# Optimization experiments

Measured on AMD Instinct MI355X. Metric: run time of the kernel, lower is better.

The kernel has to match this reference:

```python
import jax, jax.numpy as jnp
import numpy as np

N = 50000
E = 800000
IN_DIM = 256
HID = 64
HEADS = 4
OUT_DIM = 32
NEG_SLOPE = 0.2
EPS = 1e-5


def segment_softmax(logits, seg, num_segments):
    # logits: [E, H]; softmax over edges sharing the same destination node
    m = jax.ops.segment_max(logits, seg, num_segments=num_segments)
    m = jnp.where(jnp.isfinite(m), m, 0.0)
    e = jnp.exp(logits - m[seg])
    s = jax.ops.segment_sum(e, seg, num_segments=num_segments)
    return e / (s[seg] + 1e-16)


def setup_inputs() -> dict:
    key = jax.random.key(0)
    ks = jax.random.split(key, 16)
    d = {}
    d['x'] = jax.random.normal(ks[0], (N, IN_DIM), dtype=jnp.float32)
    d['edge_index'] = jax.random.randint(ks[1], (2, E), 0, N, dtype=jnp.int64)
    sc = lambda fan: 1.0 / np.sqrt(fan)
    # input transform: Linear(256->128), Linear(128->64)
    d['t1_w'] = jax.random.normal(ks[2], (IN_DIM, IN_DIM // 2), dtype=jnp.float32) * sc(IN_DIM)
    d['t1_b'] = jnp.zeros((IN_DIM // 2,), jnp.float32)
    d['t2_w'] = jax.random.normal(ks[3], (IN_DIM // 2, IN_DIM // 4), dtype=jnp.float32) * sc(IN_DIM // 2)
    d['t2_b'] = jnp.zeros((IN_DIM // 4,), jnp.float32)
    d['g1_w'] = jax.random.normal(ks[4], (IN_DIM // 4, HEADS * HID), dtype=jnp.float32) * sc(IN_DIM // 4)
    d['g1_att_src'] = jax.random.normal(ks[5], (HEADS, HID), dtype=jnp.float32) * sc(HID)
    d['g1_att_dst'] = jax.random.normal(ks[6], (HEADS, HID), dtype=jnp.float32) * sc(HID)
    d['g1_b'] = jnp.zeros((HEADS * HID,), jnp.float32)
    # GraphNorm(256)
    d['gn_w'] = jnp.ones((HEADS * HID,), jnp.float32)
    d['gn_b'] = jnp.zeros((HEADS * HID,), jnp.float32)
    d['gn_ms'] = jnp.ones((HEADS * HID,), jnp.float32)
    # GATConv 2: 256 -> 32, 1 head, no concat (mean == identity for 1 head)
    d['g2_w'] = jax.random.normal(ks[7], (HEADS * HID, OUT_DIM), dtype=jnp.float32) * sc(HEADS * HID)
    d['g2_att_src'] = jax.random.normal(ks[8], (1, OUT_DIM), dtype=jnp.float32) * sc(OUT_DIM)
    d['g2_att_dst'] = jax.random.normal(ks[9], (1, OUT_DIM), dtype=jnp.float32) * sc(OUT_DIM)
    d['g2_b'] = jnp.zeros((OUT_DIM,), jnp.float32)
    return d


def gat_conv(x, src, dst, w, att_src, att_dst, bias, n_nodes):
    heads, ch = att_src.shape
    h = (x @ w).reshape(n_nodes, heads, ch)            # [N,H,C]
    a_src = jnp.sum(h * att_src, axis=-1)              # [N,H]
    a_dst = jnp.sum(h * att_dst, axis=-1)              # [N,H]
    logits = jax.nn.leaky_relu(a_src[src] + a_dst[dst], NEG_SLOPE)  # [E,H]
    alpha = segment_softmax(logits, dst, n_nodes)      # [E,H]
    msgs = alpha[:, :, None] * h[src]                  # [E,H,C]
    out = jax.ops.segment_sum(msgs, dst, num_segments=n_nodes)  # [N,H,C]
    return out.reshape(n_nodes, heads * ch) + bias


def reference(x, edge_index, t1_w, t1_b, t2_w, t2_b,
              g1_w, g1_att_src, g1_att_dst, g1_b,
              gn_w, gn_b, gn_ms,
              g2_w, g2_att_src, g2_att_dst, g2_b):
    src, dst = edge_index[0], edge_index[1]
    # input transform (dropout inactive in eval)
    h = jax.nn.relu(x @ t1_w + t1_b)
    h = jax.nn.relu(h @ t2_w + t2_b)
    # GAT layer 1 (concat heads)
    h = gat_conv(h, src, dst, g1_w, g1_att_src, g1_att_dst, g1_b, N)
    # GraphNorm over the whole graph (batch=None -> single graph)
    mean = jnp.mean(h, axis=0)
    o = h - mean * gn_ms
    var = jnp.mean(o * o, axis=0)
    h = o / jnp.sqrt(var + EPS) * gn_w + gn_b
    h = jax.nn.elu(h)
    # GAT layer 2 (1 head, concat=False)
    h = gat_conv(h, src, dst, g2_w, g2_att_src, g2_att_dst, g2_b, N)
    return jax.nn.log_softmax(h, axis=1)
```

## Files before the change

### kernel.cpp

```cpp
#include <hip/hip_runtime.h>

#define NSLOPE 0.2f
#define GEPS 1e-5f

typedef unsigned short ushortT;
typedef __attribute__((ext_vector_type(8))) unsigned short us8;
typedef __attribute__((ext_vector_type(8))) __bf16 bf16x8;
typedef __attribute__((ext_vector_type(4))) float f32x4;

__device__ __forceinline__ float lrelu(float x) { return x >= 0.f ? x : NSLOPE * x; }
__device__ __forceinline__ ushortT f2bf(float f) {
    unsigned int u = __float_as_uint(f);
    return (ushortT)((u + 0x7fffu + ((u >> 16) & 1u)) >> 16);
}
__device__ __forceinline__ float bf2f(ushortT h) {
    return __uint_as_float((unsigned int)h << 16);
}

__global__ __launch_bounds__(256) void k_prep(
    const float* __restrict__ w1, const float* __restrict__ w2,
    const float* __restrict__ g1w, const float* __restrict__ g2w,
    ushortT* __restrict__ w1t, ushortT* __restrict__ w2t,
    ushortT* __restrict__ g1t, ushortT* __restrict__ g2t)
{
    const int i = blockIdx.x * 256 + threadIdx.x;
    if (i < 128 * 256) { const int c = i >> 8, k = i & 255; w1t[i] = f2bf(w1[k * 128 + c]); }
    if (i < 64 * 128)  { const int c = i >> 7, k = i & 127; w2t[i] = f2bf(w2[k * 64 + c]); }
    if (i < 256 * 64)  { const int c = i >> 6, k = i & 63;  g1t[i] = f2bf(g1w[k * 256 + c]); }
    if (i < 32 * 256)  { const int c = i >> 8, k = i & 255; g2t[i] = f2bf(g2w[k * 32 + c]); }
}

__global__ __launch_bounds__(256) void k_lin1(const float* __restrict__ x,
    const ushortT* __restrict__ w1t, const float* __restrict__ b1,
    ushortT* __restrict__ h1, int n)
{
    __shared__ us8 Ab[64 * 128 / 16];
    __shared__ us8 Bb[128 * 128 / 16];
    char* A = (char*)Ab; char* B = (char*)Bb;
    const int t = threadIdx.x;
    const int w = t >> 6, l = t & 63;
    const int lo = l & 15, hi = l >> 4;
    const int n0 = blockIdx.x * 64;
    const int wm = (w >> 1) * 32, wn = (w & 1) * 64;
    f32x4 acc[2][4];
    #pragma unroll
    for (int mf = 0; mf < 2; ++mf)
        #pragma unroll
        for (int nf = 0; nf < 4; ++nf) acc[mf][nf] = (f32x4){0.f, 0.f, 0.f, 0.f};

    const int arow = t >> 2, ak0 = (t & 3) * 16;
    int agn = n0 + arow; if (agn >= n) agn = n - 1;
    const int asw = (arow & 7) << 4;

    for (int kc = 0; kc < 4; ++kc) {
        __syncthreads();
        {
            ushortT tmp[16];
            const float* xp = &x[(size_t)agn * 256 + kc * 64 + ak0];
            #pragma unroll
            for (int j = 0; j < 4; ++j) {
                const float4 v = *(const float4*)(xp + j * 4);
                tmp[j*4+0] = f2bf(v.x); tmp[j*4+1] = f2bf(v.y);
                tmp[j*4+2] = f2bf(v.z); tmp[j*4+3] = f2bf(v.w);
            }
            *(us8*)(A + arow * 128 + ((ak0 * 2) ^ asw)) = *(us8*)tmp;
            *(us8*)(A + arow * 128 + ((ak0 * 2 + 16) ^ asw)) = *(us8*)(tmp + 8);
        }
        #pragma unroll
        for (int i = 0; i < 4; ++i) {
            const int idx = i * 256 + t, br = idx >> 3, bs = idx & 7;
            const us8 v = *(const us8*)&w1t[(size_t)br * 256 + kc * 64 + bs * 8];
            *(us8*)(B + br * 128 + ((bs * 16) ^ ((br & 7) << 4))) = v;
        }
        __syncthreads();
        #pragma unroll
        for (int ks = 0; ks < 2; ++ks) {
            const int koff = ks * 64 + hi * 16;
            bf16x8 af[2], bf[4];
            #pragma unroll
            for (int mf = 0; mf < 2; ++mf) {
                const int r = wm + mf * 16 + lo;
                af[mf] = *(const bf16x8*)(A + r * 128 + (koff ^ ((r & 7) << 4)));
            }
            #pragma unroll
            for (int nf = 0; nf < 4; ++nf) {
                const int r = wn + nf * 16 + lo;
                bf[nf] = *(const bf16x8*)(B + r * 128 + (koff ^ ((r & 7) << 4)));
            }
            #pragma unroll
            for (int mf = 0; mf < 2; ++mf)
                #pragma unroll
                for (int nf = 0; nf < 4; ++nf)
                    acc[mf][nf] = __builtin_amdgcn_mfma_f32_16x16x32_bf16(af[mf], bf[nf], acc[mf][nf], 0, 0, 0);
        }
    }
    #pragma unroll
    for (int nf = 0; nf < 4; ++nf) {
        const int col = wn + nf * 16 + lo;
        const float bb = b1[col];
        #pragma unroll
        for (int mf = 0; mf < 2; ++mf)
            #pragma unroll
            for (int j = 0; j < 4; ++j) {
                const int r = n0 + wm + mf * 16 + hi * 4 + j;
                if (r < n) h1[(size_t)r * 128 + col] = f2bf(fmaxf(acc[mf][nf][j] + bb, 0.f));
            }
    }
}

__global__ __launch_bounds__(256) void k_lin2(const ushortT* __restrict__ h1,
    const ushortT* __restrict__ w2t, const float* __restrict__ b2,
    ushortT* __restrict__ h2, int n)
{
    __shared__ us8 Ab[64 * 128 / 16];
    __shared__ us8 Bb[64 * 128 / 16];
    char* A = (char*)Ab; char* B = (char*)Bb;
    const int t = threadIdx.x;
    const int w = t >> 6, l = t & 63;
    const int lo = l & 15, hi = l >> 4;
    const int n0 = blockIdx.x * 64;
    const int wm = (w >> 1) * 32, wn = (w & 1) * 32;
    f32x4 acc[2][2];
    #pragma unroll
    for (int mf = 0; mf < 2; ++mf)
        #pragma unroll
        for (int nf = 0; nf < 2; ++nf) acc[mf][nf] = (f32x4){0.f, 0.f, 0.f, 0.f};

    const int arow = t >> 2, ak0 = (t & 3) * 16;
    int agn = n0 + arow; if (agn >= n) agn = n - 1;
    const int asw = (arow & 7) << 4;

    for (int kc = 0; kc < 2; ++kc) {
        __syncthreads();
        {
            const us8 v0 = *(const us8*)&h1[(size_t)agn * 128 + kc * 64 + ak0];
            const us8 v1 = *(const us8*)&h1[(size_t)agn * 128 + kc * 64 + ak0 + 8];
            *(us8*)(A + arow * 128 + ((ak0 * 2) ^ asw)) = v0;
            *(us8*)(A + arow * 128 + ((ak0 * 2 + 16) ^ asw)) = v1;
        }
        #pragma unroll
        for (int i = 0; i < 2; ++i) {
            const int idx = i * 256 + t, br = idx >> 3, bs = idx & 7;
            const us8 v = *(const us8*)&w2t[(size_t)br * 128 + kc * 64 + bs * 8];
            *(us8*)(B + br * 128 + ((bs * 16) ^ ((br & 7) << 4))) = v;
        }
        __syncthreads();
        #pragma unroll
        for (int ks = 0; ks < 2; ++ks) {
            const int koff = ks * 64 + hi * 16;
            bf16x8 af[2], bf[2];
            #pragma unroll
            for (int mf = 0; mf < 2; ++mf) {
                const int r = wm + mf * 16 + lo;
                af[mf] = *(const bf16x8*)(A + r * 128 + (koff ^ ((r & 7) << 4)));
            }
            #pragma unroll
            for (int nf = 0; nf < 2; ++nf) {
                const int r = wn + nf * 16 + lo;
                bf[nf] = *(const bf16x8*)(B + r * 128 + (koff ^ ((r & 7) << 4)));
            }
            #pragma unroll
            for (int mf = 0; mf < 2; ++mf)
                #pragma unroll
                for (int nf = 0; nf < 2; ++nf)
                    acc[mf][nf] = __builtin_amdgcn_mfma_f32_16x16x32_bf16(af[mf], bf[nf], acc[mf][nf], 0, 0, 0);
        }
    }
    #pragma unroll
    for (int nf = 0; nf < 2; ++nf) {
        const int col = wn + nf * 16 + lo;
        const float bb = b2[col];
        #pragma unroll
        for (int mf = 0; mf < 2; ++mf)
            #pragma unroll
            for (int j = 0; j < 4; ++j) {
                const int r = n0 + wm + mf * 16 + hi * 4 + j;
                if (r < n) h2[(size_t)r * 64 + col] = f2bf(fmaxf(acc[mf][nf][j] + bb, 0.f));
            }
    }
}

__global__ __launch_bounds__(256) void k_g1feat(const ushortT* __restrict__ h2,
    const ushortT* __restrict__ g1t, const float* __restrict__ attS, const float* __restrict__ attD,
    ushortT* __restrict__ hg1, float* __restrict__ a1s, float* __restrict__ a1d, int n)
{
    __shared__ us8 Ab[64 * 128 / 16];
    __shared__ us8 Bb[256 * 128 / 16];
    char* A = (char*)Ab; char* B = (char*)Bb;
    const int t = threadIdx.x;
    const int w = t >> 6, l = t & 63;
    const int lo = l & 15, hi = l >> 4;
    const int n0 = blockIdx.x * 64;
    const int wm = (w >> 1) * 32, wn = (w & 1) * 128;
    f32x4 acc[2][8];
    #pragma unroll
    for (int mf = 0; mf < 2; ++mf)
        #pragma unroll
        for (int nf = 0; nf < 8; ++nf) acc[mf][nf] = (f32x4){0.f, 0.f, 0.f, 0.f};

    {
        const int arow = t >> 2, ak0 = (t & 3) * 16;
        int agn = n0 + arow; if (agn >= n) agn = n - 1;
        const int asw = (arow & 7) << 4;
        const us8 v0 = *(const us8*)&h2[(size_t)agn * 64 + ak0];
        const us8 v1 = *(const us8*)&h2[(size_t)agn * 64 + ak0 + 8];
        *(us8*)(A + arow * 128 + ((ak0 * 2) ^ asw)) = v0;
        *(us8*)(A + arow * 128 + ((ak0 * 2 + 16) ^ asw)) = v1;
    }
    #pragma unroll
    for (int i = 0; i < 8; ++i) {
        const int idx = i * 256 + t, br = idx >> 3, bs = idx & 7;
        const us8 v = *(const us8*)&g1t[(size_t)br * 64 + bs * 8];
        *(us8*)(B + br * 128 + ((bs * 16) ^ ((br & 7) << 4))) = v;
    }
    __syncthreads();
    #pragma unroll
    for (int ks = 0; ks < 2; ++ks) {
        const int koff = ks * 64 + hi * 16;
        bf16x8 af[2];
        #pragma unroll
        for (int mf = 0; mf < 2; ++mf) {
            const int r = wm + mf * 16 + lo;
            af[mf] = *(const bf16x8*)(A + r * 128 + (koff ^ ((r & 7) << 4)));
        }
        #pragma unroll
        for (int nf = 0; nf < 8; ++nf) {
            const int r = wn + nf * 16 + lo;
            const bf16x8 bf = *(const bf16x8*)(B + r * 128 + (koff ^ ((r & 7) << 4)));
            #pragma unroll
            for (int mf = 0; mf < 2; ++mf)
                acc[mf][nf] = __builtin_amdgcn_mfma_f32_16x16x32_bf16(af[mf], bf, acc[mf][nf], 0, 0, 0);
        }
    }
    float sS[8], sD[8];
    #pragma unroll
    for (int nf = 0; nf < 8; ++nf) {
        sS[nf] = attS[wn + nf * 16 + lo];
        sD[nf] = attD[wn + nf * 16 + lo];
    }
    const int hA = wn >> 6, hB = hA + 1;
    #pragma unroll
    for (int mf = 0; mf < 2; ++mf)
        #pragma unroll
        for (int j = 0; j < 4; ++j) {
            const int r = n0 + wm + mf * 16 + hi * 4 + j;
            float pSA = 0.f, pDA = 0.f, pSB = 0.f, pDB = 0.f;
            #pragma unroll
            for (int nf = 0; nf < 4; ++nf) {
                pSA = fmaf(acc[mf][nf][j], sS[nf], pSA);
                pDA = fmaf(acc[mf][nf][j], sD[nf], pDA);
                pSB = fmaf(acc[mf][nf + 4][j], sS[nf + 4], pSB);
                pDB = fmaf(acc[mf][nf + 4][j], sD[nf + 4], pDB);
            }
            #pragma unroll
            for (int off = 1; off < 16; off <<= 1) {
                pSA += __shfl_xor(pSA, off);
                pDA += __shfl_xor(pDA, off);
                pSB += __shfl_xor(pSB, off);
                pDB += __shfl_xor(pDB, off);
            }
            if (r < n) {
                if (lo == 0) {
                    a1s[r * 4 + hA] = pSA; a1s[r * 4 + hB] = pSB;
                    a1d[r * 4 + hA] = pDA; a1d[r * 4 + hB] = pDB;
                }
                #pragma unroll
                for (int nf = 0; nf < 8; ++nf)
                    hg1[(size_t)r * 256 + wn + nf * 16 + lo] = f2bf(acc[mf][nf][j]);
            }
        }
}

__global__ __launch_bounds__(256) void k_g2feat(const float* __restrict__ out1,
    const float* __restrict__ cscale, const float* __restrict__ cshift,
    const ushortT* __restrict__ g2t, const float* __restrict__ attS, const float* __restrict__ attD,
    ushortT* __restrict__ hg2, float* __restrict__ a2s, float* __restrict__ a2d, int n)
{
    __shared__ us8 Ab[64 * 128 / 16];
    __shared__ us8 Bb[32 * 128 / 16];
    char* A = (char*)Ab; char* B = (char*)Bb;
    const int t = threadIdx.x;
    const int w = t >> 6, l = t & 63;
    const int lo = l & 15, hi = l >> 4;
    const int n0 = blockIdx.x * 64;
    const int wm = w * 16;
    f32x4 acc[2];
    acc[0] = (f32x4){0.f, 0.f, 0.f, 0.f};
    acc[1] = (f32x4){0.f, 0.f, 0.f, 0.f};

    const int arow = t >> 2, ak0 = (t & 3) * 16;
    int agn = n0 + arow; if (agn >= n) agn = n - 1;
    const int asw = (arow & 7) << 4;

    for (int kc = 0; kc < 4; ++kc) {
        __syncthreads();
        {
            ushortT tmp[16];
            const float* xp = &out1[(size_t)agn * 256 + kc * 64 + ak0];
            #pragma unroll
            for (int j = 0; j < 4; ++j) {
                float4 v = *(const float4*)(xp + j * 4);
                const float4 sc = *(const float4*)&cscale[kc * 64 + ak0 + j * 4];
                const float4 sh = *(const float4*)&cshift[kc * 64 + ak0 + j * 4];
                v.x = v.x * sc.x + sh.x; v.y = v.y * sc.y + sh.y;
                v.z = v.z * sc.z + sh.z; v.w = v.w * sc.w + sh.w;
                v.x = v.x > 0.f ? v.x : __expf(v.x) - 1.f;
                v.y = v.y > 0.f ? v.y : __expf(v.y) - 1.f;
                v.z = v.z > 0.f ? v.z : __expf(v.z) - 1.f;
                v.w = v.w > 0.f ? v.w : __expf(v.w) - 1.f;
                tmp[j*4+0] = f2bf(v.x); tmp[j*4+1] = f2bf(v.y);
                tmp[j*4+2] = f2bf(v.z); tmp[j*4+3] = f2bf(v.w);
            }
            *(us8*)(A + arow * 128 + ((ak0 * 2) ^ asw)) = *(us8*)tmp;
            *(us8*)(A + arow * 128 + ((ak0 * 2 + 16) ^ asw)) = *(us8*)(tmp + 8);
        }
        {
            const int br = t >> 3, bs = t & 7;
            const us8 v = *(const us8*)&g2t[(size_t)br * 256 + kc * 64 + bs * 8];
            *(us8*)(B + br * 128 + ((bs * 16) ^ ((br & 7) << 4))) = v;
        }
        __syncthreads();
        #pragma unroll
        for (int ks = 0; ks < 2; ++ks) {
            const int koff = ks * 64 + hi * 16;
            const int ra = wm + lo;
            const bf16x8 af = *(const bf16x8*)(A + ra * 128 + (koff ^ ((ra & 7) << 4)));
            #pragma unroll
            for (int nf = 0; nf < 2; ++nf) {
                const int r = nf * 16 + lo;
                const bf16x8 bf = *(const bf16x8*)(B + r * 128 + (koff ^ ((r & 7) << 4)));
                acc[nf] = __builtin_amdgcn_mfma_f32_16x16x32_bf16(af, bf, acc[nf], 0, 0, 0);
            }
        }
    }
    float sS[2], sD[2];
    sS[0] = attS[lo]; sS[1] = attS[16 + lo];
    sD[0] = attD[lo]; sD[1] = attD[16 + lo];
    #pragma unroll
    for (int j = 0; j < 4; ++j) {
        const int r = n0 + wm + hi * 4 + j;
        float pS = fmaf(acc[0][j], sS[0], acc[1][j] * sS[1]);
        float pD = fmaf(acc[0][j], sD[0], acc[1][j] * sD[1]);
        #pragma unroll
        for (int off = 1; off < 16; off <<= 1) {
            pS += __shfl_xor(pS, off);
            pD += __shfl_xor(pD, off);
        }
        if (r < n) {
            if (lo == 0) { a2s[r] = pS; a2d[r] = pD; }
            hg2[(size_t)r * 32 + lo] = f2bf(acc[0][j]);
            hg2[(size_t)r * 32 + 16 + lo] = f2bf(acc[1][j]);
        }
    }
}

__global__ void k_hist(const int* __restrict__ dst, int* __restrict__ deg, int e) {
    int i = blockIdx.x * 256 + threadIdx.x;
    if (i < e) atomicAdd(&deg[dst[i]], 1);
}

__global__ __launch_bounds__(256) void k_scan1(const int* __restrict__ deg, int* __restrict__ offs,
                                               int* __restrict__ bsum, int n)
{
    __shared__ int sm[256];
    const int t = threadIdx.x;
    const int i = blockIdx.x * 256 + t;
    const int v = (i < n) ? deg[i] : 0;
    sm[t] = v;
    __syncthreads();
    for (int off = 1; off < 256; off <<= 1) {
        int add = (t >= off) ? sm[t - off] : 0;
        __syncthreads();
        sm[t] += add;
        __syncthreads();
    }
    if (i < n) offs[i] = sm[t] - v;
    if (t == 255) bsum[blockIdx.x] = sm[255];
}

__global__ __launch_bounds__(256) void k_scan2(int* __restrict__ bsum, int nb) {
    __shared__ int sm[256];
    const int t = threadIdx.x;
    const int v = (t < nb) ? bsum[t] : 0;
    sm[t] = v;
    __syncthreads();
    for (int off = 1; off < 256; off <<= 1) {
        int add = (t >= off) ? sm[t - off] : 0;
        __syncthreads();
        sm[t] += add;
        __syncthreads();
    }
    if (t < nb) bsum[t] = sm[t] - v;
}

__global__ void k_scan3(int* __restrict__ offs, int* __restrict__ cursor,
                        const int* __restrict__ bsum, int n, int e) {
    int i = blockIdx.x * 256 + threadIdx.x;
    if (i < n) {
        int o = offs[i] + bsum[i >> 8];
        offs[i] = o;
        cursor[i] = o;
    }
    if (i == 0) offs[n] = e;
}

__global__ void k_scatter(const int* __restrict__ src, const int* __restrict__ dst,
                          int* __restrict__ cursor, int* __restrict__ csr, int e) {
    int i = blockIdx.x * 256 + threadIdx.x;
    if (i < e) {
        int p = atomicAdd(&cursor[dst[i]], 1);
        csr[p] = src[i];
    }
}

__global__ __launch_bounds__(256) void k_alpha1(
    const float* __restrict__ a1s, const float* __restrict__ a1d,
    const int* __restrict__ offs, const int* __restrict__ csr,
    float* __restrict__ alphaE, int n)
{
    const int l = threadIdx.x & 15;
    const int d = blockIdx.x * 16 + (threadIdx.x >> 4);
    if (d >= n) return;
    const int start = offs[d], end = offs[d + 1];
    const float4* __restrict__ a1s4 = (const float4*)a1s;
    const float4 adv = ((const float4*)a1d)[d];
    const float ad0 = adv.x, ad1 = adv.y, ad2 = adv.z, ad3 = adv.w;

    float m0 = -1e30f, m1 = -1e30f, m2 = -1e30f, m3 = -1e30f;
    float s0 = 0.f, s1 = 0.f, s2 = 0.f, s3 = 0.f;
    for (int e = start + l; e < end; e += 16) {
        const float4 av = a1s4[csr[e]];
        const float l0 = lrelu(av.x + ad0), l1 = lrelu(av.y + ad1);
        const float l2 = lrelu(av.z + ad2), l3 = lrelu(av.w + ad3);
        float nm;
        nm = fmaxf(m0, l0); s0 = s0 * __expf(m0 - nm) + __expf(l0 - nm); m0 = nm;
        nm = fmaxf(m1, l1); s1 = s1 * __expf(m1 - nm) + __expf(l1 - nm); m1 = nm;
        nm = fmaxf(m2, l2); s2 = s2 * __expf(m2 - nm) + __expf(l2 - nm); m2 = nm;
        nm = fmaxf(m3, l3); s3 = s3 * __expf(m3 - nm) + __expf(l3 - nm); m3 = nm;
    }
    for (int off = 1; off < 16; off <<= 1) {
        float om, os, nm;
        om = __shfl_xor(m0, off, 16); os = __shfl_xor(s0, off, 16);
        nm = fmaxf(m0, om); s0 = s0 * __expf(m0 - nm) + os * __expf(om - nm); m0 = nm;
        om = __shfl_xor(m1, off, 16); os = __shfl_xor(s1, off, 16);
        nm = fmaxf(m1, om); s1 = s1 * __expf(m1 - nm) + os * __expf(om - nm); m1 = nm;
        om = __shfl_xor(m2, off, 16); os = __shfl_xor(s2, off, 16);
        nm = fmaxf(m2, om); s2 = s2 * __expf(m2 - nm) + os * __expf(om - nm); m2 = nm;
        om = __shfl_xor(m3, off, 16); os = __shfl_xor(s3, off, 16);
        nm = fmaxf(m3, om); s3 = s3 * __expf(m3 - nm) + os * __expf(om - nm); m3 = nm;
    }
    const float i0 = 1.f / (s0 + 1e-16f), i1 = 1.f / (s1 + 1e-16f);
    const float i2 = 1.f / (s2 + 1e-16f), i3 = 1.f / (s3 + 1e-16f);
    for (int e = start + l; e < end; e += 16) {
        const float4 av = a1s4[csr[e]];
        float4 o;
        o.x = __expf(lrelu(av.x + ad0) - m0) * i0;
        o.y = __expf(lrelu(av.y + ad1) - m1) * i1;
        o.z = __expf(lrelu(av.z + ad2) - m2) * i2;
        o.w = __expf(lrelu(av.w + ad3) - m3) * i3;
        *(float4*)&alphaE[(size_t)e * 4] = o;
    }
}

__global__ __launch_bounds__(256) void k_pv1(
    const ushortT* __restrict__ hg1, const float* __restrict__ alphaE,
    const int* __restrict__ offs, const int* __restrict__ csr,
    const float* __restrict__ bias, float* __restrict__ out1, int n)
{
    const int lane = threadIdx.x & 63;
    const int d = blockIdx.x * 4 + (threadIdx.x >> 6);
    if (d >= n) return;
    const int start = offs[d], end = offs[d + 1];
    const int c = lane * 4;
    const int head = lane >> 4;
    float acc0 = 0.f, acc1 = 0.f, acc2 = 0.f, acc3 = 0.f;
    #pragma unroll 4
    for (int e = start; e < end; ++e) {
        const int si = csr[e];
        const float al = alphaE[(size_t)e * 4 + head];
        const ushort4 hv = *(const ushort4*)&hg1[(size_t)si * 256 + c];
        acc0 = fmaf(al, bf2f(hv.x), acc0);
        acc1 = fmaf(al, bf2f(hv.y), acc1);
        acc2 = fmaf(al, bf2f(hv.z), acc2);
        acc3 = fmaf(al, bf2f(hv.w), acc3);
    }
    const float4 bv = *(const float4*)&bias[c];
    float4 o = {acc0 + bv.x, acc1 + bv.y, acc2 + bv.z, acc3 + bv.w};
    *(float4*)&out1[(size_t)d * 256 + c] = o;
}

__global__ __launch_bounds__(256) void k_colstat(const float* __restrict__ out1,
    float* __restrict__ colsum, float* __restrict__ colsq, int n)
{
    const int t = threadIdx.x;
    float s = 0.f, q = 0.f;
    for (int r = blockIdx.x; r < n; r += gridDim.x) {
        float v = out1[(size_t)r * 256 + t];
        s += v;
        q += v * v;
    }
    atomicAdd(&colsum[t], s);
    atomicAdd(&colsq[t], q);
}

__global__ void k_norm_params(const float* __restrict__ colsum, const float* __restrict__ colsq,
    const float* __restrict__ gw, const float* __restrict__ gb, const float* __restrict__ gms,
    float* __restrict__ scale, float* __restrict__ shift, int n)
{
    const int t = threadIdx.x;
    const float invn = 1.f / (float)n;
    const float mean = colsum[t] * invn;
    const float msq = colsq[t] * invn;
    const float ms = gms[t];
    const float var = msq - 2.f * ms * mean * mean + ms * ms * mean * mean;
    const float sc = gw[t] * rsqrtf(var + GEPS);
    scale[t] = sc;
    shift[t] = gb[t] - mean * ms * sc;
}

__global__ __launch_bounds__(256) void k_alpha2(
    const float* __restrict__ a2s, const float* __restrict__ a2d,
    const int* __restrict__ offs, const int* __restrict__ csr,
    float* __restrict__ alphaE2, int n)
{
    const int l = threadIdx.x & 15;
    const int d = blockIdx.x * 16 + (threadIdx.x >> 4);
    if (d >= n) return;
    const int start = offs[d], end = offs[d + 1];
    const float adv = a2d[d];
    float m = -1e30f, s = 0.f;
    for (int e = start + l; e < end; e += 16) {
        const float lv = lrelu(a2s[csr[e]] + adv);
        const float nm = fmaxf(m, lv);
        s = s * __expf(m - nm) + __expf(lv - nm);
        m = nm;
    }
    for (int off = 1; off < 16; off <<= 1) {
        const float om = __shfl_xor(m, off, 16), os = __shfl_xor(s, off, 16);
        const float nm = fmaxf(m, om);
        s = s * __expf(m - nm) + os * __expf(om - nm);
        m = nm;
    }
    const float inv = 1.f / (s + 1e-16f);
    for (int e = start + l; e < end; e += 16)
        alphaE2[e] = __expf(lrelu(a2s[csr[e]] + adv) - m) * inv;
}

__global__ __launch_bounds__(256) void k_pv2(
    const ushortT* __restrict__ hg2, const float* __restrict__ alphaE2,
    const int* __restrict__ offs, const int* __restrict__ csr,
    const float* __restrict__ bias, float* __restrict__ out, int n)
{
    const int l = threadIdx.x & 31;
    const int d = blockIdx.x * 8 + (threadIdx.x >> 5);
    if (d >= n) return;
    const int start = offs[d], end = offs[d + 1];
    float acc = 0.f;
    #pragma unroll 4
    for (int e = start; e < end; ++e) {
        const int si = csr[e];
        const float al = alphaE2[e];
        acc = fmaf(al, bf2f(hg2[(size_t)si * 32 + l]), acc);
    }
    const float v = acc + bias[l];
    float mx = v;
    for (int off = 16; off; off >>= 1) mx = fmaxf(mx, __shfl_xor(mx, off, 32));
    float se = __expf(v - mx);
    for (int off = 16; off; off >>= 1) se += __shfl_xor(se, off, 32);
    out[(size_t)d * 32 + l] = v - mx - __logf(se);
}

extern "C" void kernel_launch(void* const* d_in, const int* in_sizes, int n_in,
                              void* d_out, int out_size, void* d_ws, size_t ws_size,
                              hipStream_t stream)
{
    const float* x    = (const float*)d_in[0];
    const int*   ei   = (const int*)d_in[1];
    const float* t1w  = (const float*)d_in[2];
    const float* t1b  = (const float*)d_in[3];
    const float* t2w  = (const float*)d_in[4];
    const float* t2b  = (const float*)d_in[5];
    const float* g1w  = (const float*)d_in[6];
    const float* g1as = (const float*)d_in[7];
    const float* g1ad = (const float*)d_in[8];
    const float* g1b  = (const float*)d_in[9];
    const float* gnw  = (const float*)d_in[10];
    const float* gnb  = (const float*)d_in[11];
    const float* gnms = (const float*)d_in[12];
    const float* g2w  = (const float*)d_in[13];
    const float* g2as = (const float*)d_in[14];
    const float* g2ad = (const float*)d_in[15];
    const float* g2b  = (const float*)d_in[16];

    const int N = in_sizes[0] / 256;
    const int E = in_sizes[1] / 2;
    const int* srcA = ei;
    const int* dstA = ei + E;

    char* ws = (char*)d_ws;
    size_t cur = 0;
    auto alloc = [&](size_t bytes) -> char* {
        char* p = ws + cur;
        cur += (bytes + 255) & ~(size_t)255;
        return p;
    };
    ushortT* h1      = (ushortT*)alloc((size_t)N * 128 * 2);
    ushortT* h2      = (ushortT*)alloc((size_t)N * 64 * 2);
    ushortT* hg1     = (ushortT*)alloc((size_t)N * 256 * 2);
    float*   a1s     = (float*)alloc((size_t)N * 4 * 4);
    float*   a1d     = (float*)alloc((size_t)N * 4 * 4);
    float*   out1    = (float*)alloc((size_t)N * 256 * 4);
    ushortT* hg2     = (ushortT*)alloc((size_t)N * 32 * 2);
    float*   a2s     = (float*)alloc((size_t)N * 4);
    float*   a2d     = (float*)alloc((size_t)N * 4);
    int*     deg     = (int*)alloc((size_t)(N + 1) * 4);
    int*     offs    = (int*)alloc((size_t)(N + 1) * 4);
    int*     cursor  = (int*)alloc((size_t)N * 4);
    int*     bsum    = (int*)alloc(1024);
    int*     csr     = (int*)alloc((size_t)E * 4);
    float*   alphaE  = (float*)alloc((size_t)E * 4 * 4);
    float*   alphaE2 = (float*)alloc((size_t)E * 4);
    float*   colsum  = (float*)alloc(1024);
    float*   colsq   = (float*)alloc(1024);
    float*   cscale  = (float*)alloc(1024);
    float*   cshift  = (float*)alloc(1024);
    ushortT* w1t     = (ushortT*)alloc(128 * 256 * 2);
    ushortT* w2t     = (ushortT*)alloc(64 * 128 * 2);
    ushortT* g1t     = (ushortT*)alloc(256 * 64 * 2);
    ushortT* g2t     = (ushortT*)alloc(32 * 256 * 2);

    hipMemsetAsync(deg, 0, (size_t)(N + 1) * 4, stream);
    hipMemsetAsync(colsum, 0, 2048, stream);

    const int EB  = (E + 255) / 256;
    const int NB  = (N + 255) / 256;
    const int B64 = (N + 63) / 64;
    const int B16 = (N + 15) / 16;
    const int B8  = (N + 7) / 8;
    const int B4  = (N + 3) / 4;

    k_prep<<<128, 256, 0, stream>>>(t1w, t2w, g1w, g2w, w1t, w2t, g1t, g2t);
    k_lin1<<<B64, 256, 0, stream>>>(x, w1t, t1b, h1, N);
    k_lin2<<<B64, 256, 0, stream>>>(h1, w2t, t2b, h2, N);
    k_g1feat<<<B64, 256, 0, stream>>>(h2, g1t, g1as, g1ad, hg1, a1s, a1d, N);
    k_hist<<<EB, 256, 0, stream>>>(dstA, deg, E);
    k_scan1<<<NB, 256, 0, stream>>>(deg, offs, bsum, N);
    k_scan2<<<1, 256, 0, stream>>>(bsum, NB);
    k_scan3<<<NB, 256, 0, stream>>>(offs, cursor, bsum, N, E);
    k_scatter<<<EB, 256, 0, stream>>>(srcA, dstA, cursor, csr, E);
    k_alpha1<<<B16, 256, 0, stream>>>(a1s, a1d, offs, csr, alphaE, N);
    k_pv1<<<B4, 256, 0, stream>>>(hg1, alphaE, offs, csr, g1b, out1, N);
    k_colstat<<<256, 256, 0, stream>>>(out1, colsum, colsq, N);
    k_norm_params<<<1, 256, 0, stream>>>(colsum, colsq, gnw, gnb, gnms, cscale, cshift, N);
    k_g2feat<<<B64, 256, 0, stream>>>(out1, cscale, cshift, g2t, g2as, g2ad, hg2, a2s, a2d, N);
    k_alpha2<<<B16, 256, 0, stream>>>(a2s, a2d, offs, csr, alphaE2, N);
    k_pv2<<<B8, 256, 0, stream>>>(hg2, alphaE2, offs, csr, g2b, (float*)d_out, N);
}
```

Baseline: 324.7 us.

## Store layer-1 GAT output in bf16 and stage edge lists in LDS

The intermediate out1 tensor (N x 256) is now written as bf16 instead of fp32. That halves the bytes written by k_pv1 and read by k_colstat and k_g2feat, and those kernels now convert on load. Separately, k_pv1 and k_pv2 stage chunks of source indices and attention weights into shared memory with one coalesced load per wavefront. This replaces the per-edge scalar broadcast loads from global memory. Rounding out1 to bf16 before GraphNorm statistics adds some precision loss.

```diff
diff --git a/kernel.cpp b/kernel.cpp
--- a/kernel.cpp
+++ b/kernel.cpp
@@ -271,7 +271,7 @@
         }
 }
 
-__global__ __launch_bounds__(256) void k_g2feat(const float* __restrict__ out1,
+__global__ __launch_bounds__(256) void k_g2feat(const ushortT* __restrict__ out1,
     const float* __restrict__ cscale, const float* __restrict__ cshift,
     const ushortT* __restrict__ g2t, const float* __restrict__ attS, const float* __restrict__ attD,
     ushortT* __restrict__ hg2, float* __restrict__ a2s, float* __restrict__ a2d, int n)
@@ -296,20 +296,15 @@
         __syncthreads();
         {
             ushortT tmp[16];
-            const float* xp = &out1[(size_t)agn * 256 + kc * 64 + ak0];
-            #pragma unroll
-            for (int j = 0; j < 4; ++j) {
-                float4 v = *(const float4*)(xp + j * 4);
-                const float4 sc = *(const float4*)&cscale[kc * 64 + ak0 + j * 4];
-                const float4 sh = *(const float4*)&cshift[kc * 64 + ak0 + j * 4];
-                v.x = v.x * sc.x + sh.x; v.y = v.y * sc.y + sh.y;
-                v.z = v.z * sc.z + sh.z; v.w = v.w * sc.w + sh.w;
-                v.x = v.x > 0.f ? v.x : __expf(v.x) - 1.f;
-                v.y = v.y > 0.f ? v.y : __expf(v.y) - 1.f;
-                v.z = v.z > 0.f ? v.z : __expf(v.z) - 1.f;
-                v.w = v.w > 0.f ? v.w : __expf(v.w) - 1.f;
-                tmp[j*4+0] = f2bf(v.x); tmp[j*4+1] = f2bf(v.y);
-                tmp[j*4+2] = f2bf(v.z); tmp[j*4+3] = f2bf(v.w);
+            const us8 v0 = *(const us8*)&out1[(size_t)agn * 256 + kc * 64 + ak0];
+            const us8 v1 = *(const us8*)&out1[(size_t)agn * 256 + kc * 64 + ak0 + 8];
+            #pragma unroll
+            for (int j = 0; j < 8; ++j) {
+                float a = bf2f(v0[j]) * cscale[kc * 64 + ak0 + j] + cshift[kc * 64 + ak0 + j];
+                float b = bf2f(v1[j]) * cscale[kc * 64 + ak0 + 8 + j] + cshift[kc * 64 + ak0 + 8 + j];
+                a = a > 0.f ? a : __expf(a) - 1.f;
+                b = b > 0.f ? b : __expf(b) - 1.f;
+                tmp[j] = f2bf(a); tmp[8 + j] = f2bf(b);
             }
             *(us8*)(A + arow * 128 + ((ak0 * 2) ^ asw)) = *(us8*)tmp;
             *(us8*)(A + arow * 128 + ((ak0 * 2 + 16) ^ asw)) = *(us8*)(tmp + 8);
@@ -465,37 +460,48 @@
 __global__ __launch_bounds__(256) void k_pv1(
     const ushortT* __restrict__ hg1, const float* __restrict__ alphaE,
     const int* __restrict__ offs, const int* __restrict__ csr,
-    const float* __restrict__ bias, float* __restrict__ out1, int n)
-{
-    const int lane = threadIdx.x & 63;
-    const int d = blockIdx.x * 4 + (threadIdx.x >> 6);
+    const float* __restrict__ bias, ushortT* __restrict__ out1, int n)
+{
+    __shared__ int sSid[4][64];
+    __shared__ float sAl[4][256];
+    const int lane = threadIdx.x & 63, w = threadIdx.x >> 6;
+    const int d = blockIdx.x * 4 + w;
     if (d >= n) return;
     const int start = offs[d], end = offs[d + 1];
     const int c = lane * 4;
     const int head = lane >> 4;
     float acc0 = 0.f, acc1 = 0.f, acc2 = 0.f, acc3 = 0.f;
-    #pragma unroll 4
-    for (int e = start; e < end; ++e) {
-        const int si = csr[e];
-        const float al = alphaE[(size_t)e * 4 + head];
-        const ushort4 hv = *(const ushort4*)&hg1[(size_t)si * 256 + c];
-        acc0 = fmaf(al, bf2f(hv.x), acc0);
-        acc1 = fmaf(al, bf2f(hv.y), acc1);
-        acc2 = fmaf(al, bf2f(hv.z), acc2);
-        acc3 = fmaf(al, bf2f(hv.w), acc3);
+    for (int base = start; base < end; base += 64) {
+        const int cnt = min(64, end - base);
+        if (lane < cnt) {
+            sSid[w][lane] = csr[base + lane];
+            *(float4*)&sAl[w][lane * 4] = *(const float4*)&alphaE[(size_t)(base + lane) * 4];
+        }
+        #pragma unroll 8
+        for (int i = 0; i < cnt; ++i) {
+            const int si = sSid[w][i];
+            const float al = sAl[w][i * 4 + head];
+            const ushort4 hv = *(const ushort4*)&hg1[(size_t)si * 256 + c];
+            acc0 = fmaf(al, bf2f(hv.x), acc0);
+            acc1 = fmaf(al, bf2f(hv.y), acc1);
+            acc2 = fmaf(al, bf2f(hv.z), acc2);
+            acc3 = fmaf(al, bf2f(hv.w), acc3);
+        }
     }
     const float4 bv = *(const float4*)&bias[c];
-    float4 o = {acc0 + bv.x, acc1 + bv.y, acc2 + bv.z, acc3 + bv.w};
-    *(float4*)&out1[(size_t)d * 256 + c] = o;
-}
-
-__global__ __launch_bounds__(256) void k_colstat(const float* __restrict__ out1,
+    ushort4 o;
+    o.x = f2bf(acc0 + bv.x); o.y = f2bf(acc1 + bv.y);
+    o.z = f2bf(acc2 + bv.z); o.w = f2bf(acc3 + bv.w);
+    *(ushort4*)&out1[(size_t)d * 256 + c] = o;
+}
+
+__global__ __launch_bounds__(256) void k_colstat(const ushortT* __restrict__ out1,
     float* __restrict__ colsum, float* __restrict__ colsq, int n)
 {
     const int t = threadIdx.x;
     float s = 0.f, q = 0.f;
     for (int r = blockIdx.x; r < n; r += gridDim.x) {
-        float v = out1[(size_t)r * 256 + t];
+        const float v = bf2f(out1[(size_t)r * 256 + t]);
         s += v;
         q += v * v;
     }
@@ -551,16 +557,25 @@
     const int* __restrict__ offs, const int* __restrict__ csr,
     const float* __restrict__ bias, float* __restrict__ out, int n)
 {
-    const int l = threadIdx.x & 31;
-    const int d = blockIdx.x * 8 + (threadIdx.x >> 5);
+    __shared__ int sSid[8][32];
+    __shared__ float sAl[8][32];
+    const int l = threadIdx.x & 31, w = threadIdx.x >> 5;
+    const int d = blockIdx.x * 8 + w;
     if (d >= n) return;
     const int start = offs[d], end = offs[d + 1];
     float acc = 0.f;
-    #pragma unroll 4
-    for (int e = start; e < end; ++e) {
-        const int si = csr[e];
-        const float al = alphaE2[e];
-        acc = fmaf(al, bf2f(hg2[(size_t)si * 32 + l]), acc);
+    for (int base = start; base < end; base += 32) {
+        const int cnt = min(32, end - base);
+        if (l < cnt) {
+            sSid[w][l] = csr[base + l];
+            sAl[w][l] = alphaE2[base + l];
+        }
+        #pragma unroll 8
+        for (int i = 0; i < cnt; ++i) {
+            const int si = sSid[w][i];
+            const float al = sAl[w][i];
+            acc = fmaf(al, bf2f(hg2[(size_t)si * 32 + l]), acc);
+        }
     }
     const float v = acc + bias[l];
     float mx = v;
@@ -609,7 +624,7 @@
     ushortT* hg1     = (ushortT*)alloc((size_t)N * 256 * 2);
     float*   a1s     = (float*)alloc((size_t)N * 4 * 4);
     float*   a1d     = (float*)alloc((size_t)N * 4 * 4);
-    float*   out1    = (float*)alloc((size_t)N * 256 * 4);
+    ushortT* out1    = (ushortT*)alloc((size_t)N * 256 * 2);
     ushortT* hg2     = (ushortT*)alloc((size_t)N * 32 * 2);
     float*   a2s     = (float*)alloc((size_t)N * 4);
     float*   a2d     = (float*)alloc((size_t)N * 4);
```

Measured after the change: 319.9 us. No clear change (-1.5%).

## Store GAT layer-1 output in bf16 and split edge loops across half-waves

Applied to the files above, without the earlier changes.

The intermediate out1 buffer changes from fp32 to bf16, which halves the traffic written by k_pv1 and read by k_colstat and k_g2feat. k_pv1 now has each lane load 8 bf16 channels and splits the edges between the two half-wavefronts, merging them with a shuffle, so more gathers are in flight. k_pv2 packs two channels per lane across 16 lanes and handles twice as many nodes per block. The cost is extra bf16 rounding of the pre-norm activations, which shifts the GraphNorm statistics slightly.

```diff
diff --git a/kernel.cpp b/kernel.cpp
--- a/kernel.cpp
+++ b/kernel.cpp
@@ -271,7 +271,7 @@
         }
 }
 
-__global__ __launch_bounds__(256) void k_g2feat(const float* __restrict__ out1,
+__global__ __launch_bounds__(256) void k_g2feat(const ushortT* __restrict__ out1,
     const float* __restrict__ cscale, const float* __restrict__ cshift,
     const ushortT* __restrict__ g2t, const float* __restrict__ attS, const float* __restrict__ attD,
     ushortT* __restrict__ hg2, float* __restrict__ a2s, float* __restrict__ a2d, int n)
@@ -296,20 +296,15 @@
         __syncthreads();
         {
             ushortT tmp[16];
-            const float* xp = &out1[(size_t)agn * 256 + kc * 64 + ak0];
-            #pragma unroll
-            for (int j = 0; j < 4; ++j) {
-                float4 v = *(const float4*)(xp + j * 4);
-                const float4 sc = *(const float4*)&cscale[kc * 64 + ak0 + j * 4];
-                const float4 sh = *(const float4*)&cshift[kc * 64 + ak0 + j * 4];
-                v.x = v.x * sc.x + sh.x; v.y = v.y * sc.y + sh.y;
-                v.z = v.z * sc.z + sh.z; v.w = v.w * sc.w + sh.w;
-                v.x = v.x > 0.f ? v.x : __expf(v.x) - 1.f;
-                v.y = v.y > 0.f ? v.y : __expf(v.y) - 1.f;
-                v.z = v.z > 0.f ? v.z : __expf(v.z) - 1.f;
-                v.w = v.w > 0.f ? v.w : __expf(v.w) - 1.f;
-                tmp[j*4+0] = f2bf(v.x); tmp[j*4+1] = f2bf(v.y);
-                tmp[j*4+2] = f2bf(v.z); tmp[j*4+3] = f2bf(v.w);
+            const us8 v0 = *(const us8*)&out1[(size_t)agn * 256 + kc * 64 + ak0];
+            const us8 v1 = *(const us8*)&out1[(size_t)agn * 256 + kc * 64 + ak0 + 8];
+            #pragma unroll
+            for (int j = 0; j < 8; ++j) {
+                float a = bf2f(v0[j]) * cscale[kc * 64 + ak0 + j] + cshift[kc * 64 + ak0 + j];
+                float b = bf2f(v1[j]) * cscale[kc * 64 + ak0 + 8 + j] + cshift[kc * 64 + ak0 + 8 + j];
+                a = a > 0.f ? a : __expf(a) - 1.f;
+                b = b > 0.f ? b : __expf(b) - 1.f;
+                tmp[j] = f2bf(a); tmp[8 + j] = f2bf(b);
             }
             *(us8*)(A + arow * 128 + ((ak0 * 2) ^ asw)) = *(us8*)tmp;
             *(us8*)(A + arow * 128 + ((ak0 * 2 + 16) ^ asw)) = *(us8*)(tmp + 8);
@@ -462,40 +457,52 @@
     }
 }
 
-__global__ __launch_bounds__(256) void k_pv1(
+__global__ __launch_bounds__(256, 8) void k_pv1(
     const ushortT* __restrict__ hg1, const float* __restrict__ alphaE,
     const int* __restrict__ offs, const int* __restrict__ csr,
-    const float* __restrict__ bias, float* __restrict__ out1, int n)
+    const float* __restrict__ bias, ushortT* __restrict__ out1, int n)
 {
     const int lane = threadIdx.x & 63;
     const int d = blockIdx.x * 4 + (threadIdx.x >> 6);
     if (d >= n) return;
     const int start = offs[d], end = offs[d + 1];
-    const int c = lane * 4;
-    const int head = lane >> 4;
-    float acc0 = 0.f, acc1 = 0.f, acc2 = 0.f, acc3 = 0.f;
+    const int cg = lane & 31;
+    const int c = cg * 8;
+    const int es = lane >> 5;
+    const int head = cg >> 3;
+    float acc[8];
+    #pragma unroll
+    for (int j = 0; j < 8; ++j) acc[j] = 0.f;
+
     #pragma unroll 4
-    for (int e = start; e < end; ++e) {
+    for (int e = start + es; e < end; e += 2) {
         const int si = csr[e];
         const float al = alphaE[(size_t)e * 4 + head];
-        const ushort4 hv = *(const ushort4*)&hg1[(size_t)si * 256 + c];
-        acc0 = fmaf(al, bf2f(hv.x), acc0);
-        acc1 = fmaf(al, bf2f(hv.y), acc1);
-        acc2 = fmaf(al, bf2f(hv.z), acc2);
-        acc3 = fmaf(al, bf2f(hv.w), acc3);
-    }
-    const float4 bv = *(const float4*)&bias[c];
-    float4 o = {acc0 + bv.x, acc1 + bv.y, acc2 + bv.z, acc3 + bv.w};
-    *(float4*)&out1[(size_t)d * 256 + c] = o;
-}
-
-__global__ __launch_bounds__(256) void k_colstat(const float* __restrict__ out1,
+        const us8 hv = *(const us8*)&hg1[(size_t)si * 256 + c];
+        #pragma unroll
+        for (int j = 0; j < 8; ++j) acc[j] = fmaf(al, bf2f(hv[j]), acc[j]);
+    }
+    #pragma unroll
+    for (int j = 0; j < 8; ++j) acc[j] += __shfl_xor(acc[j], 32);
+    if (es == 0) {
+        const float4 b0 = *(const float4*)&bias[c];
+        const float4 b1 = *(const float4*)&bias[c + 4];
+        us8 o;
+        o[0] = f2bf(acc[0] + b0.x); o[1] = f2bf(acc[1] + b0.y);
+        o[2] = f2bf(acc[2] + b0.z); o[3] = f2bf(acc[3] + b0.w);
+        o[4] = f2bf(acc[4] + b1.x); o[5] = f2bf(acc[5] + b1.y);
+        o[6] = f2bf(acc[6] + b1.z); o[7] = f2bf(acc[7] + b1.w);
+        *(us8*)&out1[(size_t)d * 256 + c] = o;
+    }
+}
+
+__global__ __launch_bounds__(256) void k_colstat(const ushortT* __restrict__ out1,
     float* __restrict__ colsum, float* __restrict__ colsq, int n)
 {
     const int t = threadIdx.x;
     float s = 0.f, q = 0.f;
     for (int r = blockIdx.x; r < n; r += gridDim.x) {
-        float v = out1[(size_t)r * 256 + t];
+        const float v = bf2f(out1[(size_t)r * 256 + t]);
         s += v;
         q += v * v;
     }
@@ -546,28 +553,34 @@
         alphaE2[e] = __expf(lrelu(a2s[csr[e]] + adv) - m) * inv;
 }
 
-__global__ __launch_bounds__(256) void k_pv2(
+__global__ __launch_bounds__(256, 8) void k_pv2(
     const ushortT* __restrict__ hg2, const float* __restrict__ alphaE2,
     const int* __restrict__ offs, const int* __restrict__ csr,
     const float* __restrict__ bias, float* __restrict__ out, int n)
 {
-    const int l = threadIdx.x & 31;
-    const int d = blockIdx.x * 8 + (threadIdx.x >> 5);
+    const int l = threadIdx.x & 15;
+    const int d = blockIdx.x * 16 + (threadIdx.x >> 4);
     if (d >= n) return;
     const int start = offs[d], end = offs[d + 1];
-    float acc = 0.f;
-    #pragma unroll 4
+    const int c = l * 2;
+    float acc0 = 0.f, acc1 = 0.f;
+    #pragma unroll 8
     for (int e = start; e < end; ++e) {
         const int si = csr[e];
         const float al = alphaE2[e];
-        acc = fmaf(al, bf2f(hg2[(size_t)si * 32 + l]), acc);
-    }
-    const float v = acc + bias[l];
-    float mx = v;
-    for (int off = 16; off; off >>= 1) mx = fmaxf(mx, __shfl_xor(mx, off, 32));
-    float se = __expf(v - mx);
-    for (int off = 16; off; off >>= 1) se += __shfl_xor(se, off, 32);
-    out[(size_t)d * 32 + l] = v - mx - __logf(se);
+        const ushort2 hv = *(const ushort2*)&hg2[(size_t)si * 32 + c];
+        acc0 = fmaf(al, bf2f(hv.x), acc0);
+        acc1 = fmaf(al, bf2f(hv.y), acc1);
+    }
+    const float v0 = acc0 + bias[c];
+    const float v1 = acc1 + bias[c + 1];
+    float mx = fmaxf(v0, v1);
+    for (int off = 1; off < 16; off <<= 1) mx = fmaxf(mx, __shfl_xor(mx, off, 16));
+    float se = __expf(v0 - mx) + __expf(v1 - mx);
+    for (int off = 1; off < 16; off <<= 1) se += __shfl_xor(se, off, 16);
+    const float ls = __logf(se);
+    float2 o = {v0 - mx - ls, v1 - mx - ls};
+    *(float2*)&out[(size_t)d * 32 + c] = o;
 }
 
 extern "C" void kernel_launch(void* const* d_in, const int* in_sizes, int n_in,
@@ -609,7 +622,7 @@
     ushortT* hg1     = (ushortT*)alloc((size_t)N * 256 * 2);
     float*   a1s     = (float*)alloc((size_t)N * 4 * 4);
     float*   a1d     = (float*)alloc((size_t)N * 4 * 4);
-    float*   out1    = (float*)alloc((size_t)N * 256 * 4);
+    ushortT* out1    = (ushortT*)alloc((size_t)N * 256 * 2);
     ushortT* hg2     = (ushortT*)alloc((size_t)N * 32 * 2);
     float*   a2s     = (float*)alloc((size_t)N * 4);
     float*   a2d     = (float*)alloc((size_t)N * 4);
@@ -636,7 +649,6 @@
     const int NB  = (N + 255) / 256;
     const int B64 = (N + 63) / 64;
     const int B16 = (N + 15) / 16;
-    const int B8  = (N + 7) / 8;
     const int B4  = (N + 3) / 4;
 
     k_prep<<<128, 256, 0, stream>>>(t1w, t2w, g1w, g2w, w1t, w2t, g1t, g2t);
@@ -654,5 +666,5 @@
     k_norm_params<<<1, 256, 0, stream>>>(colsum, colsq, gnw, gnb, gnms, cscale, cshift, N);
     k_g2feat<<<B64, 256, 0, stream>>>(out1, cscale, cshift, g2t, g2as, g2ad, hg2, a2s, a2d, N);
     k_alpha2<<<B16, 256, 0, stream>>>(a2s, a2d, offs, csr, alphaE2, N);
-    k_pv2<<<B8, 256, 0, stream>>>(hg2, alphaE2, offs, csr, g2b, (float*)d_out, N);
-}
+    k_pv2<<<B16, 256, 0, stream>>>(hg2, alphaE2, offs, csr, g2b, (float*)d_out, N);
+}
```

After: 320.5 us. No clear change (-1.3%).
